# Kernel tuning notes

Measured on AMD Instinct MI355X. Metric: run time of the kernel, lower is better.

The kernel has to match this reference:

```python
import jax, jax.numpy as jnp
import numpy as np

S, B, E, H = 50, 512, 512, 512
C_TANH = 10.0  # tanh_exploration, use_tanh=True for pointer heads


def setup_inputs() -> dict:
    key = jax.random.key(0)
    ks = iter(jax.random.split(key, 64))
    sE = 1.0 / np.sqrt(E)
    sH = 1.0 / np.sqrt(H)

    def n(shape, s=1.0):
        return jax.random.normal(next(ks), shape, dtype=jnp.float32) * s

    inp = {
        'decoder_input': n((B, E)),
        'embedded_inputs': n((S, B, E)),
        'h0': n((B, H)), 'c0': n((B, H)),
        'context': n((S, B, H)),
        'enc_h_aoi': n((S, B, E)),
        'decoder_inputs_aoi': n((S, B, H)),
        'h0_aoi': n((B, H)), 'c0_aoi': n((B, H)),
        'V_reach_mask': jnp.zeros((B, S), dtype=bool),
        # LSTMCell params (PyTorch gate order i,f,g,o)
        'W_ih': n((4 * H, E), sE), 'W_hh': n((4 * H, H), sH),
        'b_ih': n((4 * H,), sH), 'b_hh': n((4 * H,), sH),
        'W_ih_a': n((4 * H, E), sE), 'W_hh_a': n((4 * H, H), sH),
        'b_ih_a': n((4 * H,), sH), 'b_hh_a': n((4 * H,), sH),
    }
    # Attention modules: pointer (p), pointer_aoi (pa), glimpse (g), glimpse_aoi (ga)
    for tag in ('p', 'pa', 'g', 'ga'):
        inp['Wq_' + tag] = n((H, H), sH)
        inp['bq_' + tag] = n((H,), sH)
        inp['Wr_' + tag] = n((H, H), sH)  # Conv1d(dim,dim,1) == per-position linear
        inp['br_' + tag] = n((H,), sH)
        inp['v_' + tag] = n((H,), sH)
    return inp


def _decoder(decoder_input, embedded_inputs, h0, c0, context, enc_h_aoi,
             decoder_inputs_aoi, h0_aoi, c0_aoi, V_reach_mask,
             W_ih, W_hh, b_ih, b_hh, W_ih_a, W_hh_a, b_ih_a, b_hh_a,
             Wq_p, bq_p, Wr_p, br_p, v_p, Wq_pa, bq_pa, Wr_pa, br_pa, v_pa,
             Wq_g, bq_g, Wr_g, br_g, v_g, Wq_ga, bq_ga, Wr_ga, br_ga, v_ga):
    arangeB = jnp.arange(B)

    def proj_ref(Wr, br, ctx):  # ctx [S,B,H] -> e [B,H,S]
        return jnp.einsum('hd,sbd->bhs', Wr, ctx) + br[None, :, None]

    # project_ref of each Attention depends only on the fixed context -> hoist out of loop
    e_g = proj_ref(Wr_g, br_g, context)
    e_p = proj_ref(Wr_p, br_p, context)
    e_ga = proj_ref(Wr_ga, br_ga, decoder_inputs_aoi)
    e_pa = proj_ref(Wr_pa, br_pa, decoder_inputs_aoi)

    def lstm_cell(x, h, c, Wih, Whh, bih, bhh):
        g = x @ Wih.T + bih + h @ Whh.T + bhh
        i, f, gc, o = jnp.split(g, 4, axis=1)
        c2 = jax.nn.sigmoid(f) * c + jax.nn.sigmoid(i) * jnp.tanh(gc)
        return jax.nn.sigmoid(o) * jnp.tanh(c2), c2

    def attn_logits(q_in, Wq, bq, e, v):  # q_in [B,H], e [B,H,S] -> [B,S]
        q = q_in @ Wq.T + bq
        return jnp.einsum('h,bhs->bs', v, jnp.tanh(q[:, :, None] + e))

    def mask_modify(m):  # if a row is all-True, free the last column
        all_true = m.all(axis=1)
        return m.at[:, -1].set(jnp.where(all_true, False, m[:, -1]))

    def branch(x, h, c, Wih, Whh, bih, bhh, Wq_gl, bq_gl, e_gl, v_gl,
               Wq_pt, bq_pt, e_pt, v_pt, mask):
        h2, c2 = lstm_cell(x, h, c, Wih, Whh, bih, bhh)
        g_l = h2
        # n_glimpses = 1
        lg = attn_logits(g_l, Wq_gl, bq_gl, e_gl, v_gl)
        lg = jnp.where(mask, -jnp.inf, lg)
        g_l = jnp.einsum('bhs,bs->bh', e_gl, jax.nn.softmax(lg, axis=1))
        lp = attn_logits(g_l, Wq_pt, bq_pt, e_pt, v_pt)
        lp = C_TANH * jnp.tanh(lp)  # pointer uses use_tanh=True
        lp = jnp.where(mask, -jnp.inf, lp)
        return lp, h2, c2

    mask0 = mask_modify(V_reach_mask)  # check_mask at step 0

    def step(carry, t):
        h, c, ha, ca, mask, idxs, x, xa = carry
        upd = mask_modify(mask.at[arangeB, idxs].set(True))  # update_mask
        mask = jnp.where(t == 0, mask, upd)
        lp, h, c = branch(x, h, c, W_ih, W_hh, b_ih, b_hh,
                          Wq_g, bq_g, e_g, v_g, Wq_p, bq_p, e_p, v_p, mask)
        lpa, ha, ca = branch(xa, ha, ca, W_ih_a, W_hh_a, b_ih_a, b_hh_a,
                             Wq_ga, bq_ga, e_ga, v_ga, Wq_pa, bq_pa, e_pa, v_pa, mask)
        log_p = jax.nn.log_softmax(lp, axis=1) + 0.1 * jax.nn.log_softmax(lpa, axis=1)
        idxs = jnp.argmax(jnp.exp(log_p), axis=1)  # greedy decode
        x = embedded_inputs[idxs, arangeB]   # gather next decoder input [B,E]
        xa = enc_h_aoi[idxs, arangeB]
        return (h, c, ha, ca, mask, idxs, x, xa), (log_p, idxs)

    init = (h0, c0, h0_aoi, c0_aoi, mask0, jnp.zeros((B,), dtype=jnp.int32),
            decoder_input, decoder_input)  # decoder_input_aoi = decoder_input.clone()
    _, (log_ps, sels) = jax.lax.scan(step, init, jnp.arange(S))
    return jnp.transpose(log_ps, (1, 0, 2)), jnp.transpose(sels, (1, 0))


def reference(decoder_input, embedded_inputs, h0, c0, context, enc_h_aoi,
              decoder_inputs_aoi, h0_aoi, c0_aoi, V_reach_mask,
              W_ih, W_hh, b_ih, b_hh, W_ih_a, W_hh_a, b_ih_a, b_hh_a,
              Wq_p, bq_p, Wr_p, br_p, v_p, Wq_pa, bq_pa, Wr_pa, br_pa, v_pa,
              Wq_g, bq_g, Wr_g, br_g, v_g, Wq_ga, bq_ga, Wr_ga, br_ga, v_ga):
    return _decoder(decoder_input, embedded_inputs, h0, c0, context, enc_h_aoi,
                    decoder_inputs_aoi, h0_aoi, c0_aoi, V_reach_mask,
                    W_ih, W_hh, b_ih, b_hh, W_ih_a, W_hh_a, b_ih_a, b_hh_a,
                    Wq_p, bq_p, Wr_p, br_p, v_p, Wq_pa, bq_pa, Wr_pa, br_pa, v_pa,
                    Wq_g, bq_g, Wr_g, br_g, v_g, Wq_ga, bq_ga, Wr_ga, br_ga, v_ga)
```

## Files before the change

### kernel.cpp

```cpp
#include <hip/hip_runtime.h>
#include <math.h>


#define S_LEN 50
#define BATCH 512
#define HDIM  512
#define H4    2048
#define BH    (BATCH*HDIM)
#define BS    (BATCH*S_LEN)
#define KSPQ  4
#define MASK50 0x0003FFFFFFFFFFFFULL

typedef unsigned short u16;
typedef __attribute__((ext_vector_type(8))) short bf16x8;
typedef __attribute__((ext_vector_type(4))) float f32x4;

__device__ __forceinline__ float wave_sum(float v){
  #pragma unroll
  for (int o=32;o;o>>=1) v += __shfl_xor(v,o);
  return v;
}
__device__ __forceinline__ float wave_max(float v){
  #pragma unroll
  for (int o=32;o;o>>=1) v = fmaxf(v,__shfl_xor(v,o));
  return v;
}
__device__ __forceinline__ float tanh_fast(float x){
  float t = __expf(2.0f*x);
  return 1.0f - 2.0f*__builtin_amdgcn_rcpf(t + 1.0f);
}
__device__ __forceinline__ float sigmoid_fast(float x){
  return __builtin_amdgcn_rcpf(1.0f + __expf(-x));
}
__device__ __forceinline__ u16 f2b(float f){
  unsigned u = __float_as_uint(f);
  unsigned r = (u + 0x7fffu + ((u>>16)&1u)) >> 16;
  return (u16)r;
}
__device__ __forceinline__ float b2f(u16 h){ return __uint_as_float(((unsigned)h)<<16); }

struct MArgs {
  const u16* A[4]; const u16* W[4]; const float* bias[4]; void* C[4];
  int M, N, K, lda, ksplit, out_bf16;
};

__global__ __launch_bounds__(256, 2) void mfma_gemm(MArgs g) {
  const int z = blockIdx.z;
  const u16* __restrict__ A = g.A[z];
  const u16* __restrict__ W = g.W[z];
  const float* __restrict__ bias = g.bias[z];
  const int N = g.N, K = g.K, lda = g.lda;
  const int mtile = blockIdx.y / g.ksplit;
  const int ksp   = blockIdx.y % g.ksplit;
  const int m0 = mtile*128, n0 = blockIdx.x*128;
  const int kc = K / g.ksplit;
  const int kbeg = ksp*kc, kend = kbeg+kc;

  __shared__ __align__(16) u16 sh[2*128*88];
  u16* As = sh;
  u16* Bs = sh + 128*88;

  const int tid = threadIdx.x;
  const int wave = tid>>6, lane = tid&63;
  const int wm = (wave>>1)*64, wn = (wave&1)*64;
  const int m16 = lane&15, quad = lane>>4;

  f32x4 acc[4][4];
  #pragma unroll
  for (int i=0;i<4;i++)
    #pragma unroll
    for (int j=0;j<4;j++) acc[i][j] = (f32x4){0.f,0.f,0.f,0.f};

  for (int kt = kbeg; kt < kend; kt += 64) {
    uint4 av[4], wv[4];
    #pragma unroll
    for (int it=0; it<4; it++){
      int idx = tid + it*256;
      int r = idx>>3, c = idx&7;
      av[it] = *(const uint4*)(A + (size_t)(m0+r)*lda + kt + c*8);
      wv[it] = *(const uint4*)(W + (size_t)(n0+r)*K + kt + c*8);
    }
    __syncthreads();
    #pragma unroll
    for (int it=0; it<4; it++){
      int idx = tid + it*256;
      int r = idx>>3, c = idx&7;
      *(uint4*)&As[r*88 + c*8] = av[it];
      *(uint4*)&Bs[r*88 + c*8] = wv[it];
    }
    __syncthreads();
    #pragma unroll
    for (int ks=0; ks<2; ks++){
      bf16x8 af[4], bfr[4];
      #pragma unroll
      for (int i=0;i<4;i++) af[i] = *(const bf16x8*)&As[(wm + i*16 + m16)*88 + ks*32 + quad*8];
      #pragma unroll
      for (int j=0;j<4;j++) bfr[j] = *(const bf16x8*)&Bs[(wn + j*16 + m16)*88 + ks*32 + quad*8];
      #pragma unroll
      for (int i=0;i<4;i++)
        #pragma unroll
        for (int j=0;j<4;j++)
          acc[i][j] = __builtin_amdgcn_mfma_f32_16x16x32_bf16(af[i], bfr[j], acc[i][j], 0, 0, 0);
    }
  }

  if (g.out_bf16) {
    u16* C = (u16*)g.C[z];
    __syncthreads();
    #pragma unroll
    for (int i=0;i<4;i++){
      #pragma unroll
      for (int j=0;j<4;j++){
        int cc = wn + j*16 + m16;
        float bv = bias ? bias[n0 + cc] : 0.0f;
        #pragma unroll
        for (int r=0;r<4;r++)
          sh[(wm + i*16 + quad*4 + r)*128 + cc] = f2b(acc[i][j][r] + bv);
      }
    }
    __syncthreads();
    #pragma unroll
    for (int k=0;k<8;k++){
      int idx = tid + k*256;
      int row = idx>>4, c = idx&15;
      *(uint4*)(C + (size_t)(m0+row)*N + n0 + c*8) = *(const uint4*)&sh[row*128 + c*8];
    }
  } else {
    float* C = (float*)g.C[z] + (size_t)ksp*g.M*N;
    float* shf = (float*)sh;
    __syncthreads();
    if (wm == 0){
      #pragma unroll
      for (int i=0;i<4;i++){
        int mb = i*16 + quad*4;
        #pragma unroll
        for (int j=0;j<4;j++){
          int cc = wn + j*16 + m16;
          float bv = bias ? bias[n0 + cc] : 0.0f;
          #pragma unroll
          for (int r=0;r<4;r++) shf[(mb+r)*128 + cc] = acc[i][j][r] + bv;
        }
      }
    }
    __syncthreads();
    #pragma unroll
    for (int k=0;k<8;k++){
      int idx = tid + k*256;
      int row = idx>>5, c = idx&31;
      *(float4*)(C + (size_t)(m0 + row)*N + n0 + c*4) = *(const float4*)&shf[row*128 + c*4];
    }
    __syncthreads();
    if (wm == 64){
      #pragma unroll
      for (int i=0;i<4;i++){
        int mb = i*16 + quad*4;
        #pragma unroll
        for (int j=0;j<4;j++){
          int cc = wn + j*16 + m16;
          float bv = bias ? bias[n0 + cc] : 0.0f;
          #pragma unroll
          for (int r=0;r<4;r++) shf[(mb+r)*128 + cc] = acc[i][j][r] + bv;
        }
      }
    }
    __syncthreads();
    #pragma unroll
    for (int k=0;k<8;k++){
      int idx = tid + k*256;
      int row = idx>>5, c = idx&31;
      *(float4*)(C + (size_t)(m0 + 64 + row)*N + n0 + c*4) = *(const float4*)&shf[row*128 + c*4];
    }
  }
}

struct F2BJobs { const float* s[8]; u16* d[8]; int n4; };

__global__ void f2b_multi(F2BJobs J){
  const float* __restrict__ src = J.s[blockIdx.y];
  u16* __restrict__ dst = J.d[blockIdx.y];
  int i = blockIdx.x*blockDim.x + threadIdx.x;
  if (i >= J.n4) return;
  float4 v = *(const float4*)(src + (size_t)i*4);
  ushort4 o; o.x=f2b(v.x); o.y=f2b(v.y); o.z=f2b(v.z); o.w=f2b(v.w);
  *(ushort4*)(dst + (size_t)i*4) = o;
}

__global__ void remap2_kernel(const float* __restrict__ srcA, u16* __restrict__ dstA,
                              const float* __restrict__ srcB, u16* __restrict__ dstB){
  const float* __restrict__ src = blockIdx.y ? srcB : srcA;
  u16* __restrict__ dst = blockIdx.y ? dstB : dstA;
  int i = blockIdx.x*blockDim.x + threadIdx.x;
  if (i >= (S_LEN*BATCH*HDIM)/4) return;
  int elem = i*4;
  int s = elem >> 18;
  int b = (elem >> 9) & 511;
  int h = elem & 511;
  float4 v = *(const float4*)(src + (size_t)s*BATCH*HDIM + (size_t)b*HDIM + h);
  ushort4 o; o.x=f2b(v.x); o.y=f2b(v.y); o.z=f2b(v.z); o.w=f2b(v.w);
  *(ushort4*)(dst + ((size_t)b*S_LEN + s)*HDIM + h) = o;
}

__global__ void init_kernel(const float* __restrict__ h0, const float* __restrict__ c0,
                            const float* __restrict__ h0a, const float* __restrict__ c0a,
                            const float* __restrict__ dec, const unsigned char* __restrict__ vmask,
                            u16* __restrict__ h_bf, float* __restrict__ c_ws,
                            u16* __restrict__ x_bf, u16* __restrict__ xa_bf,
                            int* __restrict__ mask){
  for (int i = blockIdx.x*blockDim.x + threadIdx.x; i < BH; i += gridDim.x*blockDim.x) {
    h_bf[i]=f2b(h0[i]); h_bf[BH+i]=f2b(h0a[i]);
    c_ws[i]=c0[i];      c_ws[BH+i]=c0a[i];
    u16 d = f2b(dec[i]);
    x_bf[i]=d; xa_bf[i]=d;
    if (i < BS) mask[i] = vmask[i] ? 1 : 0;
  }
}

__global__ __launch_bounds__(64) void mask_fix_kernel(int* __restrict__ mask){
  int b = blockIdx.x, lane = threadIdx.x;
  int mv = (lane < S_LEN) ? mask[b*S_LEN+lane] : 1;
  unsigned long long bal = __ballot(mv != 0);
  if ((bal & MASK50) == MASK50 && lane == 49) mask[b*S_LEN+49] = 0;
}

__global__ void gates_kernel(const float* __restrict__ g_ws,
                             const float* __restrict__ b_ih, const float* __restrict__ b_hh,
                             const float* __restrict__ b_ih_a, const float* __restrict__ b_hh_a,
                             u16* __restrict__ h_bf, float* __restrict__ c_ws){
  int i = blockIdx.x*blockDim.x + threadIdx.x;
  if (i >= 2*BH) return;
  int z = i / BH, r = i % BH;
  int b = r >> 9, j = r & 511;
  const float* gA = g_ws + (size_t)(2*z+0)*BATCH*H4 + (size_t)b*H4;
  const float* gB = g_ws + (size_t)(2*z+1)*BATCH*H4 + (size_t)b*H4;
  const float* bi = z ? b_ih_a : b_ih;
  const float* bh = z ? b_hh_a : b_hh;
  float gi = gA[j]      + gB[j]      + bi[j]      + bh[j];
  float gf = gA[512+j]  + gB[512+j]  + bi[512+j]  + bh[512+j];
  float gg = gA[1024+j] + gB[1024+j] + bi[1024+j] + bh[1024+j];
  float go = gA[1536+j] + gB[1536+j] + bi[1536+j] + bh[1536+j];
  float cp = c_ws[i];
  float c2 = sigmoid_fast(gf)*cp + sigmoid_fast(gi)*tanh_fast(gg);
  float h2 = sigmoid_fast(go)*tanh_fast(c2);
  c_ws[i] = c2; h_bf[i] = f2b(h2);
}

__global__ __launch_bounds__(512) void glimpse_kernel(
    const float* __restrict__ qpart,
    const float* __restrict__ bq_g, const float* __restrict__ bq_ga,
    const u16* __restrict__ e_g, const u16* __restrict__ e_ga,
    const float* __restrict__ v_g, const float* __restrict__ v_ga,
    const int* __restrict__ mask, u16* __restrict__ gl_ws){
  int z = blockIdx.y, b = blockIdx.x, tid = threadIdx.x;
  const u16* e = (z ? e_ga : e_g) + (size_t)b*S_LEN*HDIM;
  const float* v  = z ? v_ga : v_g;
  const float* bq = z ? bq_ga : bq_g;
  const float* qp = qpart + (size_t)z*KSPQ*BH + (size_t)b*HDIM;
  __shared__ float lg_sh[64], p_sh[64];
  int w = tid>>6, lane = tid&63;
  int h0 = lane*8;
  float qreg[8], vreg[8];
  #pragma unroll
  for (int ii=0; ii<8; ii++){
    int h = h0+ii;
    float q = bq[h];
    #pragma unroll
    for (int p=0;p<KSPQ;p++) q += qp[(size_t)p*BH + h];
    qreg[ii]=q; vreg[ii]=v[h];
  }
  for (int s = w; s < S_LEN; s += 8) {
    uint4 ev = *(const uint4*)(e + (size_t)s*HDIM + h0);
    const u16* pe = (const u16*)&ev;
    float acc = 0.0f;
    #pragma unroll
    for (int ii=0; ii<8; ii++) acc += vreg[ii]*tanh_fast(qreg[ii] + b2f(pe[ii]));
    acc = wave_sum(acc);
    if (lane==0) lg_sh[s] = mask[b*S_LEN+s] ? -INFINITY : acc;
  }
  __syncthreads();
  if (tid < 64) {
    float val = (tid < S_LEN) ? lg_sh[tid] : -INFINITY;
    float mx = wave_max(val);
    float ex = (tid < S_LEN) ? expf(val - mx) : 0.0f;
    float sm = wave_sum(ex);
    if (tid < S_LEN) p_sh[tid] = ex / sm;
  }
  __syncthreads();
  float acc = 0.0f;
  for (int s=0;s<S_LEN;s++) acc += p_sh[s]*b2f(e[(size_t)s*HDIM + tid]);
  gl_ws[(size_t)z*BH + (size_t)b*HDIM + tid] = f2b(acc);
}

__global__ __launch_bounds__(512) void pointer_combine_kernel(
    const float* __restrict__ q2part,
    const float* __restrict__ bq_p, const float* __restrict__ bq_pa,
    const u16* __restrict__ e_p, const u16* __restrict__ e_pa,
    const float* __restrict__ v_p, const float* __restrict__ v_pa,
    int* __restrict__ mask,
    const u16* __restrict__ emb_bf, const u16* __restrict__ ench_bf,
    u16* __restrict__ x_bf, u16* __restrict__ xa_bf,
    float* __restrict__ out, int t){
  int b = blockIdx.x, tid = threadIdx.x;
  int w = tid>>6, lane = tid&63;
  int z = w>>2, wz = w&3;
  __shared__ float sh_q2[2][HDIM];
  __shared__ float sh_lp[2][64];
  __shared__ int idx_sh;

  #pragma unroll
  for (int zz=0; zz<2; zz++){
    const float* qp = q2part + (size_t)zz*KSPQ*BH + (size_t)b*HDIM;
    float a2 = (zz ? bq_pa : bq_p)[tid];
    #pragma unroll
    for (int p=0;p<KSPQ;p++) a2 += qp[(size_t)p*BH + tid];
    sh_q2[zz][tid] = a2;
  }
  __syncthreads();

  const u16* ep = (z ? e_pa : e_p) + (size_t)b*S_LEN*HDIM;
  const float* vp = z ? v_pa : v_p;
  int h0 = lane*8;
  float q2r[8], vpr[8];
  #pragma unroll
  for (int ii=0; ii<8; ii++){ q2r[ii]=sh_q2[z][h0+ii]; vpr[ii]=vp[h0+ii]; }
  for (int s = wz; s < S_LEN; s += 4) {
    uint4 ev = *(const uint4*)(ep + (size_t)s*HDIM + h0);
    const u16* pe = (const u16*)&ev;
    float acc = 0.0f;
    #pragma unroll
    for (int ii=0; ii<8; ii++) acc += vpr[ii]*tanh_fast(q2r[ii] + b2f(pe[ii]));
    acc = wave_sum(acc);
    if (lane==0) sh_lp[z][s] = mask[b*S_LEN+s] ? -INFINITY : 10.0f*tanh_fast(acc);
  }
  __syncthreads();

  if (tid < 64) {
    float a  = (lane < S_LEN) ? sh_lp[0][lane] : -INFINITY;
    float ca = (lane < S_LEN) ? sh_lp[1][lane] : -INFINITY;
    float m1 = wave_max(a);
    float l1 = logf(wave_sum((lane < S_LEN) ? expf(a - m1) : 0.0f));
    float m2 = wave_max(ca);
    float l2 = logf(wave_sum((lane < S_LEN) ? expf(ca - m2) : 0.0f));
    float logp = (a - m1 - l1) + 0.1f * (ca - m2 - l2);
    if (lane < S_LEN) out[(size_t)b*(S_LEN*S_LEN) + t*S_LEN + lane] = fmaxf(logp, -1e30f);
    float vv = (lane < S_LEN) ? logp : -INFINITY;
    int bi = lane;
    #pragma unroll
    for (int o=32;o;o>>=1) {
      float ov = __shfl_xor(vv, o); int oi = __shfl_xor(bi, o);
      if (ov > vv || (ov == vv && oi < bi)) { vv = ov; bi = oi; }
    }
    int idx = bi;
    if (lane == 0) { out[(size_t)BATCH*S_LEN*S_LEN + b*S_LEN + t] = (float)idx; idx_sh = idx; }
    int mv = 1;
    if (lane < S_LEN) { mv = mask[b*S_LEN+lane]; if (lane==idx) mv = 1; mask[b*S_LEN+lane] = mv; }
    unsigned long long bal = __ballot(mv != 0);
    if ((bal & MASK50) == MASK50 && lane == 49) mask[b*S_LEN+49] = 0;
  }
  __syncthreads();

  int idx = idx_sh;
  x_bf[(size_t)b*HDIM + tid]  = emb_bf[((size_t)idx*BATCH + b)*HDIM + tid];
  xa_bf[(size_t)b*HDIM + tid] = ench_bf[((size_t)idx*BATCH + b)*HDIM + tid];
}

extern "C" void kernel_launch(void* const* d_in, const int* in_sizes, int n_in,
                              void* d_out, int out_size, void* d_ws, size_t ws_size,
                              hipStream_t stream) {
  (void)in_sizes; (void)n_in; (void)out_size; (void)ws_size;
  const float* dec    = (const float*)d_in[0];
  const float* emb    = (const float*)d_in[1];
  const float* h0     = (const float*)d_in[2];
  const float* c0     = (const float*)d_in[3];
  const float* ctx    = (const float*)d_in[4];
  const float* ench   = (const float*)d_in[5];
  const float* dia    = (const float*)d_in[6];
  const float* h0a    = (const float*)d_in[7];
  const float* c0a    = (const float*)d_in[8];
  const unsigned char* vmask = (const unsigned char*)d_in[9];
  const float* W_ih   = (const float*)d_in[10];
  const float* W_hh   = (const float*)d_in[11];
  const float* b_ih   = (const float*)d_in[12];
  const float* b_hh   = (const float*)d_in[13];
  const float* W_ih_a = (const float*)d_in[14];
  const float* W_hh_a = (const float*)d_in[15];
  const float* b_ih_a = (const float*)d_in[16];
  const float* b_hh_a = (const float*)d_in[17];
  const float* Wq_p  = (const float*)d_in[18];
  const float* bq_p  = (const float*)d_in[19];
  const float* Wr_p  = (const float*)d_in[20];
  const float* br_p  = (const float*)d_in[21];
  const float* v_p   = (const float*)d_in[22];
  const float* Wq_pa = (const float*)d_in[23];
  const float* bq_pa = (const float*)d_in[24];
  const float* Wr_pa = (const float*)d_in[25];
  const float* br_pa = (const float*)d_in[26];
  const float* v_pa  = (const float*)d_in[27];
  const float* Wq_g  = (const float*)d_in[28];
  const float* bq_g  = (const float*)d_in[29];
  const float* Wr_g  = (const float*)d_in[30];
  const float* br_g  = (const float*)d_in[31];
  const float* v_g   = (const float*)d_in[32];
  const float* Wq_ga = (const float*)d_in[33];
  const float* bq_ga = (const float*)d_in[34];
  const float* Wr_ga = (const float*)d_in[35];
  const float* br_ga = (const float*)d_in[36];
  const float* v_ga  = (const float*)d_in[37];

  char* base = (char*)d_ws;
  size_t off = 0;
  auto carve = [&](size_t bytes)->char*{ char* p = base + off; off += (bytes + 255) & ~(size_t)255; return p; };

  const size_t E_BYTES = (size_t)BS*HDIM*2;
  u16* e_g   = (u16*)carve(E_BYTES);
  u16* e_p   = (u16*)carve(E_BYTES);
  u16* e_ga  = (u16*)carve(E_BYTES);
  u16* e_pa  = (u16*)carve(E_BYTES);
  char* scratch = carve(2*E_BYTES);
  u16* A_ctx  = (u16*)scratch;
  u16* A_dia  = (u16*)(scratch + E_BYTES);
  u16* emb_bf  = A_ctx;
  u16* ench_bf = A_dia;
  u16* Wih_bf  = (u16*)carve((size_t)H4*HDIM*2);
  u16* Whh_bf  = (u16*)carve((size_t)H4*HDIM*2);
  u16* Wiha_bf = (u16*)carve((size_t)H4*HDIM*2);
  u16* Whha_bf = (u16*)carve((size_t)H4*HDIM*2);
  u16* Wqg_bf  = (u16*)carve((size_t)BH*2);
  u16* Wqga_bf = (u16*)carve((size_t)BH*2);
  u16* Wqp_bf  = (u16*)carve((size_t)BH*2);
  u16* Wqpa_bf = (u16*)carve((size_t)BH*2);
  u16* Wrg_bf  = (u16*)carve((size_t)BH*2);
  u16* Wrp_bf  = (u16*)carve((size_t)BH*2);
  u16* Wrga_bf = (u16*)carve((size_t)BH*2);
  u16* Wrpa_bf = (u16*)carve((size_t)BH*2);
  u16* x_bf    = (u16*)carve((size_t)BH*2);
  u16* xa_bf   = (u16*)carve((size_t)BH*2);
  u16* h_bf    = (u16*)carve((size_t)2*BH*2);
  float* c_ws  = (float*)carve((size_t)2*BH*4);
  float* g_ws  = (float*)carve((size_t)4*BATCH*H4*4);
  u16* gl      = (u16*)carve((size_t)2*BH*2);
  float* q_ws  = (float*)carve((size_t)2*KSPQ*BH*4);
  float* q2_ws = (float*)carve((size_t)2*KSPQ*BH*4);
  int*   mask  = (int*)carve((size_t)BS*4);
  float* out   = (float*)d_out;

  init_kernel<<<1024, 256, 0, stream>>>(h0, c0, h0a, c0a, dec, vmask,
                                        h_bf, c_ws, x_bf, xa_bf, mask);
  mask_fix_kernel<<<BATCH, 64, 0, stream>>>(mask);

  const int RB = ((S_LEN*BATCH*HDIM/4)+255)/256;
  remap2_kernel<<<dim3(RB,2), 256, 0, stream>>>(ctx, A_ctx, dia, A_dia);

  const int NW4 = H4*HDIM/4, NWQ = BH/4;
  F2BJobs jw{};
  jw.s[0]=W_ih; jw.d[0]=Wih_bf;  jw.s[1]=W_hh; jw.d[1]=Whh_bf;
  jw.s[2]=W_ih_a; jw.d[2]=Wiha_bf; jw.s[3]=W_hh_a; jw.d[3]=Whha_bf;
  jw.n4 = NW4;
  f2b_multi<<<dim3((NW4+255)/256,4), 256, 0, stream>>>(jw);

  F2BJobs jq{};
  jq.s[0]=Wq_g;  jq.d[0]=Wqg_bf;  jq.s[1]=Wq_ga; jq.d[1]=Wqga_bf;
  jq.s[2]=Wq_p;  jq.d[2]=Wqp_bf;  jq.s[3]=Wq_pa; jq.d[3]=Wqpa_bf;
  jq.s[4]=Wr_g;  jq.d[4]=Wrg_bf;  jq.s[5]=Wr_p;  jq.d[5]=Wrp_bf;
  jq.s[6]=Wr_ga; jq.d[6]=Wrga_bf; jq.s[7]=Wr_pa; jq.d[7]=Wrpa_bf;
  jq.n4 = NWQ;
  f2b_multi<<<dim3((NWQ+255)/256,8), 256, 0, stream>>>(jq);

  MArgs pa{};
  pa.A[0]=A_ctx; pa.A[1]=A_ctx; pa.A[2]=A_dia; pa.A[3]=A_dia;
  pa.W[0]=Wrg_bf; pa.W[1]=Wrp_bf; pa.W[2]=Wrga_bf; pa.W[3]=Wrpa_bf;
  pa.bias[0]=br_g; pa.bias[1]=br_p; pa.bias[2]=br_ga; pa.bias[3]=br_pa;
  pa.C[0]=e_g; pa.C[1]=e_p; pa.C[2]=e_ga; pa.C[3]=e_pa;
  pa.M=BS; pa.N=HDIM; pa.K=HDIM; pa.lda=HDIM; pa.ksplit=1; pa.out_bf16=1;
  mfma_gemm<<<dim3(4,200,4), 256, 0, stream>>>(pa);

  const int NE = S_LEN*BATCH*HDIM/4;
  F2BJobs je{};
  je.s[0]=emb; je.d[0]=emb_bf; je.s[1]=ench; je.d[1]=ench_bf;
  je.n4 = NE;
  f2b_multi<<<dim3((NE+255)/256,2), 256, 0, stream>>>(je);

  MArgs la{};
  la.A[0]=x_bf; la.A[1]=h_bf; la.A[2]=xa_bf; la.A[3]=h_bf+BH;
  la.W[0]=Wih_bf; la.W[1]=Whh_bf; la.W[2]=Wiha_bf; la.W[3]=Whha_bf;
  la.bias[0]=la.bias[1]=la.bias[2]=la.bias[3]=nullptr;
  la.C[0]=g_ws; la.C[1]=g_ws+(size_t)BATCH*H4; la.C[2]=g_ws+2*(size_t)BATCH*H4; la.C[3]=g_ws+3*(size_t)BATCH*H4;
  la.M=BATCH; la.N=H4; la.K=HDIM; la.lda=HDIM; la.ksplit=1; la.out_bf16=0;

  MArgs qg{};
  qg.A[0]=h_bf; qg.A[1]=h_bf+BH;
  qg.W[0]=Wqg_bf; qg.W[1]=Wqga_bf;
  qg.bias[0]=qg.bias[1]=qg.bias[2]=qg.bias[3]=nullptr;
  qg.C[0]=q_ws; qg.C[1]=q_ws+(size_t)KSPQ*BH;
  qg.M=BATCH; qg.N=HDIM; qg.K=HDIM; qg.lda=HDIM; qg.ksplit=KSPQ; qg.out_bf16=0;

  MArgs qp{};
  qp.A[0]=gl; qp.A[1]=gl+BH;
  qp.W[0]=Wqp_bf; qp.W[1]=Wqpa_bf;
  qp.bias[0]=qp.bias[1]=qp.bias[2]=qp.bias[3]=nullptr;
  qp.C[0]=q2_ws; qp.C[1]=q2_ws+(size_t)KSPQ*BH;
  qp.M=BATCH; qp.N=HDIM; qp.K=HDIM; qp.lda=HDIM; qp.ksplit=KSPQ; qp.out_bf16=0;

  for (int t = 0; t < S_LEN; ++t) {
    mfma_gemm<<<dim3(16,4,4), 256, 0, stream>>>(la);
    gates_kernel<<<(2*BH+255)/256, 256, 0, stream>>>(g_ws, b_ih, b_hh, b_ih_a, b_hh_a, h_bf, c_ws);
    mfma_gemm<<<dim3(4,4*KSPQ,2), 256, 0, stream>>>(qg);
    glimpse_kernel<<<dim3(BATCH,2), 512, 0, stream>>>(q_ws, bq_g, bq_ga, e_g, e_ga, v_g, v_ga, mask, gl);
    mfma_gemm<<<dim3(4,4*KSPQ,2), 256, 0, stream>>>(qp);
    pointer_combine_kernel<<<BATCH, 512, 0, stream>>>(
        q2_ws, bq_p, bq_pa, e_p, e_pa, v_p, v_pa,
        mask, emb_bf, ench_bf, x_bf, xa_bf, out, t);
  }
}
```

Measured before the change: 5.321 ms.

## Fold pointer query projection into precomputed glimpse features, drop per-step GEMM

Uses linearity of the glimpse weighted sum to precompute F = e_g·Wq_p^T (and the aoi variant) once before the loop, so each step's glimpse kernel directly produces the pointer query as a probability-weighted sum of F plus bias. This removes the per-step split-K query GEMM and the partial-sum reduction in the pointer kernel. In exchange it adds one large upfront GEMM, two extra bf16 feature buffers, and an additional bf16 rounding of the projected features.

```diff
diff --git a/kernel.cpp b/kernel.cpp
--- a/kernel.cpp
+++ b/kernel.cpp
@@ -249,7 +249,9 @@
     const float* __restrict__ bq_g, const float* __restrict__ bq_ga,
     const u16* __restrict__ e_g, const u16* __restrict__ e_ga,
     const float* __restrict__ v_g, const float* __restrict__ v_ga,
-    const int* __restrict__ mask, u16* __restrict__ gl_ws){
+    const u16* __restrict__ F_m, const u16* __restrict__ F_a,
+    const float* __restrict__ bq_p, const float* __restrict__ bq_pa,
+    const int* __restrict__ mask, float* __restrict__ q2_ws){
   int z = blockIdx.y, b = blockIdx.x, tid = threadIdx.x;
   const u16* e = (z ? e_ga : e_g) + (size_t)b*S_LEN*HDIM;
   const float* v  = z ? v_ga : v_g;
@@ -285,14 +287,14 @@
     if (tid < S_LEN) p_sh[tid] = ex / sm;
   }
   __syncthreads();
-  float acc = 0.0f;
-  for (int s=0;s<S_LEN;s++) acc += p_sh[s]*b2f(e[(size_t)s*HDIM + tid]);
-  gl_ws[(size_t)z*BH + (size_t)b*HDIM + tid] = f2b(acc);
+  const u16* F = (z ? F_a : F_m) + (size_t)b*S_LEN*HDIM;
+  float acc = (z ? bq_pa : bq_p)[tid];
+  for (int s=0;s<S_LEN;s++) acc += p_sh[s]*b2f(F[(size_t)s*HDIM + tid]);
+  q2_ws[(size_t)z*BH + (size_t)b*HDIM + tid] = acc;
 }
 
 __global__ __launch_bounds__(512) void pointer_combine_kernel(
-    const float* __restrict__ q2part,
-    const float* __restrict__ bq_p, const float* __restrict__ bq_pa,
+    const float* __restrict__ q2_ws,
     const u16* __restrict__ e_p, const u16* __restrict__ e_pa,
     const float* __restrict__ v_p, const float* __restrict__ v_pa,
     int* __restrict__ mask,
@@ -302,26 +304,16 @@
   int b = blockIdx.x, tid = threadIdx.x;
   int w = tid>>6, lane = tid&63;
   int z = w>>2, wz = w&3;
-  __shared__ float sh_q2[2][HDIM];
   __shared__ float sh_lp[2][64];
   __shared__ int idx_sh;
-
-  #pragma unroll
-  for (int zz=0; zz<2; zz++){
-    const float* qp = q2part + (size_t)zz*KSPQ*BH + (size_t)b*HDIM;
-    float a2 = (zz ? bq_pa : bq_p)[tid];
-    #pragma unroll
-    for (int p=0;p<KSPQ;p++) a2 += qp[(size_t)p*BH + tid];
-    sh_q2[zz][tid] = a2;
-  }
-  __syncthreads();
 
   const u16* ep = (z ? e_pa : e_p) + (size_t)b*S_LEN*HDIM;
   const float* vp = z ? v_pa : v_p;
   int h0 = lane*8;
   float q2r[8], vpr[8];
+  const float* q2g = q2_ws + (size_t)z*BH + (size_t)b*HDIM + h0;
   #pragma unroll
-  for (int ii=0; ii<8; ii++){ q2r[ii]=sh_q2[z][h0+ii]; vpr[ii]=vp[h0+ii]; }
+  for (int ii=0; ii<8; ii++){ q2r[ii]=q2g[ii]; vpr[ii]=vp[h0+ii]; }
   for (int s = wz; s < S_LEN; s += 4) {
     uint4 ev = *(const uint4*)(ep + (size_t)s*HDIM + h0);
     const u16* pe = (const u16*)&ev;
@@ -415,6 +407,8 @@
   u16* e_p   = (u16*)carve(E_BYTES);
   u16* e_ga  = (u16*)carve(E_BYTES);
   u16* e_pa  = (u16*)carve(E_BYTES);
+  u16* F_m   = (u16*)carve(E_BYTES);
+  u16* F_a   = (u16*)carve(E_BYTES);
   char* scratch = carve(2*E_BYTES);
   u16* A_ctx  = (u16*)scratch;
   u16* A_dia  = (u16*)(scratch + E_BYTES);
@@ -437,9 +431,8 @@
   u16* h_bf    = (u16*)carve((size_t)2*BH*2);
   float* c_ws  = (float*)carve((size_t)2*BH*4);
   float* g_ws  = (float*)carve((size_t)4*BATCH*H4*4);
-  u16* gl      = (u16*)carve((size_t)2*BH*2);
   float* q_ws  = (float*)carve((size_t)2*KSPQ*BH*4);
-  float* q2_ws = (float*)carve((size_t)2*KSPQ*BH*4);
+  float* q2_ws = (float*)carve((size_t)2*BH*4);
   int*   mask  = (int*)carve((size_t)BS*4);
   float* out   = (float*)d_out;
 
@@ -473,6 +466,14 @@
   pa.M=BS; pa.N=HDIM; pa.K=HDIM; pa.lda=HDIM; pa.ksplit=1; pa.out_bf16=1;
   mfma_gemm<<<dim3(4,200,4), 256, 0, stream>>>(pa);
 
+  MArgs fa{};
+  fa.A[0]=e_g; fa.A[1]=e_ga;
+  fa.W[0]=Wqp_bf; fa.W[1]=Wqpa_bf;
+  fa.bias[0]=fa.bias[1]=nullptr;
+  fa.C[0]=F_m; fa.C[1]=F_a;
+  fa.M=BS; fa.N=HDIM; fa.K=HDIM; fa.lda=HDIM; fa.ksplit=1; fa.out_bf16=1;
+  mfma_gemm<<<dim3(4,200,2), 256, 0, stream>>>(fa);
+
   const int NE = S_LEN*BATCH*HDIM/4;
   F2BJobs je{};
   je.s[0]=emb; je.d[0]=emb_bf; je.s[1]=ench; je.d[1]=ench_bf;
@@ -493,21 +494,15 @@
   qg.C[0]=q_ws; qg.C[1]=q_ws+(size_t)KSPQ*BH;
   qg.M=BATCH; qg.N=HDIM; qg.K=HDIM; qg.lda=HDIM; qg.ksplit=KSPQ; qg.out_bf16=0;
 
-  MArgs qp{};
-  qp.A[0]=gl; qp.A[1]=gl+BH;
-  qp.W[0]=Wqp_bf; qp.W[1]=Wqpa_bf;
-  qp.bias[0]=qp.bias[1]=qp.bias[2]=qp.bias[3]=nullptr;
-  qp.C[0]=q2_ws; qp.C[1]=q2_ws+(size_t)KSPQ*BH;
-  qp.M=BATCH; qp.N=HDIM; qp.K=HDIM; qp.lda=HDIM; qp.ksplit=KSPQ; qp.out_bf16=0;
-
   for (int t = 0; t < S_LEN; ++t) {
     mfma_gemm<<<dim3(16,4,4), 256, 0, stream>>>(la);
     gates_kernel<<<(2*BH+255)/256, 256, 0, stream>>>(g_ws, b_ih, b_hh, b_ih_a, b_hh_a, h_bf, c_ws);
     mfma_gemm<<<dim3(4,4*KSPQ,2), 256, 0, stream>>>(qg);
-    glimpse_kernel<<<dim3(BATCH,2), 512, 0, stream>>>(q_ws, bq_g, bq_ga, e_g, e_ga, v_g, v_ga, mask, gl);
-    mfma_gemm<<<dim3(4,4*KSPQ,2), 256, 0, stream>>>(qp);
+    glimpse_kernel<<<dim3(BATCH,2), 512, 0, stream>>>(
+        q_ws, bq_g, bq_ga, e_g, e_ga, v_g, v_ga,
+        F_m, F_a, bq_p, bq_pa, mask, q2_ws);
     pointer_combine_kernel<<<BATCH, 512, 0, stream>>>(
-        q2_ws, bq_p, bq_pa, e_p, e_pa, v_p, v_pa,
+        q2_ws, e_p, e_pa, v_p, v_pa,
         mask, emb_bf, ench_bf, x_bf, xa_bf, out, t);
   }
 }
```

New measurement: 4.905 ms. 1.08x faster.
